# Kernel optimization log

Hardware: AMD Instinct MI355X
Metric: run time of the kernel (lower is better)

Reference implementation:

```python
import jax, jax.numpy as jnp
import numpy as np

H, HW, B, C = 8, 64, 2, 2048  # num_heads, head_width, batch, seq_len
INIT_SCALE = 0.01
C64 = jnp.complex64


def setup_inputs() -> dict:
    key = jax.random.key(0)
    ks = jax.random.split(key, 7)
    x = jax.random.normal(ks[0], (B, C, H * HW), jnp.float32)
    W_Q = jax.random.normal(ks[1], (H, HW, HW), jnp.float32) * INIT_SCALE
    W_K = jax.random.normal(ks[2], (H, HW, HW), jnp.float32) * INIT_SCALE
    W_V = jax.random.normal(ks[3], (H, HW, HW), jnp.float32) * INIT_SCALE
    theta = jax.random.normal(ks[4], (H, HW), jnp.float32) * INIT_SCALE
    # gamma schedule: 1 - 10^linspace(-6, -2, H) (non-trainable)
    log_range = jnp.arange(H, dtype=jnp.float32) / (H - 1)
    gamma = (1.0 - 10.0 ** (-6.0 + 4.0 * log_range)).astype(jnp.float32)
    target_norm = jnp.ones((H,), jnp.float32)
    qk_scale = jnp.float32(HW ** 0.5)
    W_O = jax.random.normal(ks[5], (H, HW, H * HW), jnp.float32) * INIT_SCALE
    W_G = jax.random.normal(ks[6], (H, HW, H, HW), jnp.float32) * INIT_SCALE
    return {"x": x, "W_Q": W_Q, "W_K": W_K, "W_V": W_V, "theta": theta,
            "gamma": gamma, "target_norm": target_norm, "qk_scale": qk_scale,
            "W_O": W_O, "W_G": W_G}


def reference(x, W_Q, W_K, W_V, theta, gamma, target_norm, qk_scale, W_O, W_G):
    b, c, _ = x.shape
    # decay mask D[h, i, j] = gamma_h^(i-j) for i >= j else 0
    n = jnp.arange(c, dtype=jnp.float32)
    delta = n[:, None] - n[None, :]                       # [C, C]
    causal = delta >= 0
    expo = jnp.where(causal, delta, 0.0)
    D = jnp.where(causal[None], gamma[:, None, None] ** expo[None], 0.0)  # [H,C,C]
    # complex rotary phase Theta[h, c, i] = exp(i * c * theta[h, i])
    Theta = jnp.exp(1j * n[None, :, None] * theta[:, None, :]).astype(C64)  # [H,C,HW]
    x_head = x.reshape(b, c, H, HW).astype(C64)
    Q = jnp.einsum('hij,bchi->bhcj', W_Q.astype(C64), x_head) * Theta
    K = jnp.einsum('hij,bchi->bhcj', W_K.astype(C64), x_head) * jnp.conj(Theta)
    V = jnp.einsum('hij,bchi->bhcj', W_V.astype(C64), x_head)
    QK = jnp.einsum('bhci,bhdi->bhcd', Q, K) / qk_scale.astype(C64)  # [B,H,C,C]
    QKD = QK * D.astype(C64)
    out_head = jnp.einsum('bhcd,bhdi->bchi', QKD, V)       # [B,C,H,HW]
    # per-head L2 normalization (norm of complex vector is real)
    norm = jnp.sqrt(jnp.sum(jnp.abs(out_head) ** 2, axis=-1, keepdims=True))
    out_head = out_head / norm.astype(C64)
    # NOTE: torch code computes einsum(out_head, target_norm) into a dead variable;
    # it does not affect the returned output, so it is omitted here.
    gating = jnp.einsum('bchi,hijk->bcjk', out_head, W_G.astype(C64))  # [B,C,H,HW]
    out_head = out_head * gating / (1.0 + jnp.exp(-2.0 * gating))
    output = jnp.einsum('bchi,hik->bck', out_head, W_O.astype(C64))    # [B,C,H*HW] complex
    return output
```

## Files before the change

### kernel.cpp

```cpp
#include <hip/hip_runtime.h>
#include <cstdint>
#include <cstddef>

#define B_  2
#define H_  8
#define C_  2048
#define HW_ 64
#define HD_ 512
#define N1_ 2097152

typedef __attribute__((ext_vector_type(8))) short short8;
typedef __attribute__((ext_vector_type(4))) short short4v;
typedef __attribute__((ext_vector_type(4))) float f32x4;
typedef __attribute__((ext_vector_type(4))) int   int4v;
typedef unsigned short us;

static __device__ inline us f2bf(float f) {
    unsigned u = __builtin_bit_cast(unsigned, f);
    u = u + 0x7FFFu + ((u >> 16) & 1u);
    return (us)(u >> 16);
}
static __device__ inline us f2bf_t(float f) {
    return (us)(__builtin_bit_cast(unsigned, f) >> 16);
}
static __device__ inline float bf2f(us s) {
    unsigned u = ((unsigned)s) << 16;
    return __builtin_bit_cast(float, u);
}
static __device__ inline f32x4 mfma16(short8 a, short8 b, f32x4 c) {
    return __builtin_amdgcn_mfma_f32_16x16x32_bf16(a, b, c, 0, 0, 0);
}
static __device__ inline short8 negbf(short8 v) {
    int4v u = __builtin_bit_cast(int4v, v);
    u ^= (int)0x80008000;
    return __builtin_bit_cast(short8, u);
}
static __device__ inline short8 lds_frag(const us* p) {
    short4v a = *(const short4v*)p;
    short4v b = *(const short4v*)(p + 4);
    return __builtin_shufflevector(a, b, 0, 1, 2, 3, 4, 5, 6, 7);
}
static __device__ inline short8 lds_fragg(const us* p) {
    short4v a = *(const short4v*)p;
    short4v b = *(const short4v*)(p + 16);
    return __builtin_shufflevector(a, b, 0, 1, 2, 3, 4, 5, 6, 7);
}
static __device__ inline void pkhl(float a, float b, unsigned &hw, unsigned &lw) {
    us ha = f2bf_t(a), hb = f2bf_t(b);
    hw = (unsigned)ha | ((unsigned)hb << 16);
    float la = a - bf2f(ha), lb = b - bf2f(hb);
    lw = (unsigned)f2bf_t(la) | ((unsigned)f2bf_t(lb) << 16);
}
static __device__ inline short8 bcs8(unsigned a, unsigned b, unsigned c, unsigned d) {
    int4v v = {(int)a, (int)b, (int)c, (int)d};
    return __builtin_bit_cast(short8, v);
}

__global__ __launch_bounds__(256) void proj_kernel(
    const float* __restrict__ x, const float* __restrict__ WQ,
    const float* __restrict__ WK, const float* __restrict__ WV,
    const float* __restrict__ theta,
    us* __restrict__ Qch, us* __restrict__ Qcl,
    us* __restrict__ K1h, us* __restrict__ K1l,
    us* __restrict__ VTh, us* __restrict__ VTl)
{
    __shared__ float smem[3 * 64 * 68 + 32 * 68];
    float* sWT = smem;
    float* sx  = smem + 3 * 64 * 68;
    int tid = threadIdx.x;
    int bh = blockIdx.y; int h = bh & 7;
    int c0 = blockIdx.x * 32;
    for (int t = tid; t < 1024; t += 256) {
        int j4 = (t & 15) * 4, i = t >> 4;
        float4 wq = *(const float4*)&WQ[(h * 64 + i) * 64 + j4];
        float4 wk = *(const float4*)&WK[(h * 64 + i) * 64 + j4];
        float4 wv = *(const float4*)&WV[(h * 64 + i) * 64 + j4];
        sWT[(j4 + 0) * 68 + i] = wq.x; sWT[(j4 + 1) * 68 + i] = wq.y;
        sWT[(j4 + 2) * 68 + i] = wq.z; sWT[(j4 + 3) * 68 + i] = wq.w;
        sWT[64 * 68 + (j4 + 0) * 68 + i] = wk.x; sWT[64 * 68 + (j4 + 1) * 68 + i] = wk.y;
        sWT[64 * 68 + (j4 + 2) * 68 + i] = wk.z; sWT[64 * 68 + (j4 + 3) * 68 + i] = wk.w;
        sWT[2 * 64 * 68 + (j4 + 0) * 68 + i] = wv.x; sWT[2 * 64 * 68 + (j4 + 1) * 68 + i] = wv.y;
        sWT[2 * 64 * 68 + (j4 + 2) * 68 + i] = wv.z; sWT[2 * 64 * 68 + (j4 + 3) * 68 + i] = wv.w;
    }
    for (int t = tid; t < 512; t += 256) {
        int i4 = (t & 15) * 4, c = t >> 4;
        *(float4*)&sx[c * 68 + i4] =
            *(const float4*)&x[((size_t)((bh >> 3) * C_ + c0 + c)) * HD_ + h * 64 + i4];
    }
    __syncthreads();
    int j = tid & 63, cg = tid >> 6;
    float aq[8] = {}, ak[8] = {}, av[8] = {};
    const float* pw0 = &sWT[j * 68];
    const float* pw1 = &sWT[64 * 68 + j * 68];
    const float* pw2 = &sWT[2 * 64 * 68 + j * 68];
    const float* px  = &sx[cg * 8 * 68];
    #pragma unroll 2
    for (int i0 = 0; i0 < 64; i0 += 4) {
        float4 w0 = *(const float4*)(pw0 + i0);
        float4 w1 = *(const float4*)(pw1 + i0);
        float4 w2 = *(const float4*)(pw2 + i0);
        #pragma unroll
        for (int cc = 0; cc < 8; ++cc) {
            float4 xv = *(const float4*)(px + cc * 68 + i0);
            aq[cc] += xv.x * w0.x + xv.y * w0.y + xv.z * w0.z + xv.w * w0.w;
            ak[cc] += xv.x * w1.x + xv.y * w1.y + xv.z * w1.z + xv.w * w1.w;
            av[cc] += xv.x * w2.x + xv.y * w2.y + xv.z * w2.z + xv.w * w2.w;
        }
    }
    float th = theta[h * 64 + j];
    #pragma unroll
    for (int cc = 0; cc < 8; ++cc) {
        int c = c0 + cg * 8 + cc;
        float sn, cs;
        sincosf((float)c * th, &sn, &cs);
        float qr = aq[cc] * cs, qi = aq[cc] * sn;
        float kr = ak[cc] * cs, nki = ak[cc] * sn;
        size_t rq = ((size_t)bh * C_ + c) * 128;
        us h0;
        h0 = f2bf(qr);  Qch[rq + j]      = h0; Qcl[rq + j]      = f2bf(qr  - bf2f(h0));
        h0 = f2bf(qi);  Qch[rq + 64 + j] = h0; Qcl[rq + 64 + j] = f2bf(qi  - bf2f(h0));
        h0 = f2bf(kr);  K1h[rq + j]      = h0; K1l[rq + j]      = f2bf(kr  - bf2f(h0));
        h0 = f2bf(nki); K1h[rq + 64 + j] = h0; K1l[rq + 64 + j] = f2bf(nki - bf2f(h0));
    }
    __syncthreads();
    float* T0 = smem;
    #pragma unroll
    for (int cc = 0; cc < 8; ++cc)
        T0[j * 33 + cg * 8 + cc] = av[cc];
    __syncthreads();
    int cc2 = tid & 31, jg = tid >> 5;
    #pragma unroll
    for (int jj = 0; jj < 8; ++jj) {
        int jr = jg * 8 + jj;
        float v = T0[jr * 33 + cc2];
        us hh = f2bf(v);
        size_t o = ((size_t)bh * 64 + jr) * C_ + c0 + cc2;
        VTh[o] = hh;
        VTl[o] = f2bf(v - bf2f(hh));
    }
}

__global__ __launch_bounds__(256, 3) void retention_kernel(
    const us* __restrict__ Qch, const us* __restrict__ Qcl,
    const us* __restrict__ K1h, const us* __restrict__ K1l,
    const us* __restrict__ VTh, const us* __restrict__ VTl,
    float* __restrict__ Pbuf,
    const float* __restrict__ gamma, const float* __restrict__ qk_scale)
{
    constexpr int SPV = 68;
    constexpr int SPK = 132;
    constexpr int PLV = 64 * SPV;
    constexpr int PLK = 64 * SPK;
    __shared__ us smem[2 * PLK + 2 * PLV];
    us* sKh = smem;
    us* sKl = smem + PLK;
    us* sVh = smem + 2 * PLK;
    us* sVl = smem + 2 * PLK + PLV;

    const int tid = threadIdx.x;
    const int w = tid >> 6, lane = tid & 63;
    const int ln = lane & 15, quad = lane >> 4;
    const int r = (int)blockIdx.x >> 4, bh = (int)blockIdx.x & 15;
    const int h = bh & 7;
    int qt, klo, slot;
    if (r == 0)       { qt = 15; klo = 0;  slot = 15; }
    else if (r == 1)  { qt = 31; klo = 16; slot = 47; }
    else if (r <= 17) { qt = 14 + r; klo = 0; slot = 16 + 2 * (qt - 16); }
    else {
        int u = r - 18, s = 15 - (u >> 1);
        if ((u & 1) == 0) { qt = s - 1;  klo = 0;  slot = qt; }
        else              { qt = 15 + s; klo = 16; slot = 17 + 2 * (qt - 16); }
    }
    const int khi = (qt >= 16 && klo == 0) ? 15 : qt;
    const int qc0 = qt * 64;
    const float lg = log2f(gamma[h]);
    const float inv_scale = 1.0f / qk_scale[0];
    const int qloc = w * 16 + ln;
    const float rowl = exp2f(lg * (float)qloc);
    const float e16  = exp2f(-16.0f * lg);
    float colq[4];
    #pragma unroll
    for (int r2 = 0; r2 < 4; ++r2)
        colq[r2] = exp2f(-lg * (float)(quad * 4 + r2));

    short8 Qh[4], Ql[4];
    {
        size_t qrow = ((size_t)bh * C_ + qc0 + w * 16 + ln) * 128;
        #pragma unroll
        for (int ck = 0; ck < 4; ++ck) {
            size_t off = qrow + ck * 32 + quad * 8;
            Qh[ck] = *(const short8*)(Qch + off);
            Ql[ck] = *(const short8*)(Qcl + off);
        }
    }
    f32x4 zz = {0.0f, 0.0f, 0.0f, 0.0f};
    f32x4 Or[4], Oi[4];
    #pragma unroll
    for (int it = 0; it < 4; ++it) { Or[it] = zz; Oi[it] = zz; }

    const size_t vtb = (size_t)bh * 64 * C_;
    const int krow_s = tid >> 2, kseg = (tid & 3) * 32;
    const int vi = tid >> 2, vseg = (tid & 3) * 16;

    for (int kt = klo; kt <= khi; ++kt) {
        const int kc0 = kt * 64;
        __syncthreads();
        {
            const size_t kb = ((size_t)bh * C_ + kc0 + krow_s) * 128 + kseg;
            const us* gh = K1h + kb;
            const us* gl = K1l + kb;
            us* dkh = &sKh[krow_s * SPK + kseg];
            us* dkl = &sKl[krow_s * SPK + kseg];
            #pragma unroll
            for (int m = 0; m < 4; ++m) {
                short8 a = *(const short8*)(gh + m * 8);
                *(short4v*)(dkh + m * 8)     = __builtin_shufflevector(a, a, 0, 1, 2, 3);
                *(short4v*)(dkh + m * 8 + 4) = __builtin_shufflevector(a, a, 4, 5, 6, 7);
                a = *(const short8*)(gl + m * 8);
                *(short4v*)(dkl + m * 8)     = __builtin_shufflevector(a, a, 0, 1, 2, 3);
                *(short4v*)(dkl + m * 8 + 4) = __builtin_shufflevector(a, a, 4, 5, 6, 7);
            }
            size_t g = vtb + (size_t)vi * C_ + kc0 + vseg;
            short8 a = *(const short8*)(VTh + g);
            short8 bq = *(const short8*)(VTh + g + 8);
            *(short4v*)&sVh[vi * SPV + vseg]      = __builtin_shufflevector(a, a, 0, 1, 2, 3);
            *(short4v*)&sVh[vi * SPV + vseg + 4]  = __builtin_shufflevector(a, a, 4, 5, 6, 7);
            *(short4v*)&sVh[vi * SPV + vseg + 8]  = __builtin_shufflevector(bq, bq, 0, 1, 2, 3);
            *(short4v*)&sVh[vi * SPV + vseg + 12] = __builtin_shufflevector(bq, bq, 4, 5, 6, 7);
            a  = *(const short8*)(VTl + g);
            bq = *(const short8*)(VTl + g + 8);
            *(short4v*)&sVl[vi * SPV + vseg]      = __builtin_shufflevector(a, a, 0, 1, 2, 3);
            *(short4v*)&sVl[vi * SPV + vseg + 4]  = __builtin_shufflevector(a, a, 4, 5, 6, 7);
            *(short4v*)&sVl[vi * SPV + vseg + 8]  = __builtin_shufflevector(bq, bq, 0, 1, 2, 3);
            *(short4v*)&sVl[vi * SPV + vseg + 12] = __builtin_shufflevector(bq, bq, 4, 5, 6, 7);
        }
        __syncthreads();
        const float tf = exp2f(lg * (float)(qc0 - kc0)) * inv_scale;
        const bool diag = (kt == qt);
        float snt = tf * rowl;
        #pragma unroll
        for (int half = 0; half < 2; ++half) {
            unsigned WRH[2][2], WRL[2][2], WIH[2][2], WIL[2][2];
            #pragma unroll
            for (int n2 = 0; n2 < 2; ++n2) {
                const int nt = half * 2 + n2;
                const int kr = (nt * 16 + ln) * SPK;
                short8 Kh[4], Kl[4];
                #pragma unroll
                for (int ck = 0; ck < 4; ++ck) {
                    Kh[ck] = lds_frag(&sKh[kr + ck * 32 + quad * 8]);
                    Kl[ck] = lds_frag(&sKl[kr + ck * 32 + quad * 8]);
                }
                f32x4 sr = zz, si = zz;
                #pragma unroll
                for (int ck = 0; ck < 4; ++ck) {
                    sr = mfma16(Kh[ck], Qh[ck], sr);
                    sr = mfma16(Kl[ck], Qh[ck], sr);
                    sr = mfma16(Kh[ck], Ql[ck], sr);
                }
                short8 nKh2 = negbf(Kh[2]), nKh3 = negbf(Kh[3]);
                short8 nKl2 = negbf(Kl[2]), nKl3 = negbf(Kl[3]);
                si = mfma16(nKh2, Qh[0], si); si = mfma16(nKl2, Qh[0], si); si = mfma16(nKh2, Ql[0], si);
                si = mfma16(nKh3, Qh[1], si); si = mfma16(nKl3, Qh[1], si); si = mfma16(nKh3, Ql[1], si);
                si = mfma16(Kh[0], Qh[2], si); si = mfma16(Kl[0], Qh[2], si); si = mfma16(Kh[0], Ql[2], si);
                si = mfma16(Kh[1], Qh[3], si); si = mfma16(Kl[1], Qh[3], si); si = mfma16(Kh[1], Ql[3], si);
                float ar[4], ai[4];
                #pragma unroll
                for (int r2 = 0; r2 < 4; ++r2) {
                    float wv = snt * colq[r2];
                    if (diag && (qloc < nt * 16 + quad * 4 + r2)) wv = 0.0f;
                    ar[r2] = sr[r2] * wv;
                    ai[r2] = si[r2] * wv;
                }
                pkhl(ar[0], ar[1], WRH[n2][0], WRL[n2][0]);
                pkhl(ar[2], ar[3], WRH[n2][1], WRL[n2][1]);
                pkhl(ai[0], ai[1], WIH[n2][0], WIL[n2][0]);
                pkhl(ai[2], ai[3], WIH[n2][1], WIL[n2][1]);
                snt *= e16;
            }
            short8 SRH = bcs8(WRH[0][0], WRH[0][1], WRH[1][0], WRH[1][1]);
            short8 SRL = bcs8(WRL[0][0], WRL[0][1], WRL[1][0], WRL[1][1]);
            short8 SIH = bcs8(WIH[0][0], WIH[0][1], WIH[1][0], WIH[1][1]);
            short8 SIL = bcs8(WIL[0][0], WIL[0][1], WIL[1][0], WIL[1][1]);
            #pragma unroll
            for (int it = 0; it < 4; ++it) {
                int vb = (it * 16 + ln) * SPV + half * 32 + quad * 4;
                short8 Vh = lds_fragg(&sVh[vb]);
                short8 Vl = lds_fragg(&sVl[vb]);
                Or[it] = mfma16(SRH, Vh, Or[it]);
                Or[it] = mfma16(SRH, Vl, Or[it]);
                Or[it] = mfma16(SRL, Vh, Or[it]);
                Oi[it] = mfma16(SIH, Vh, Oi[it]);
                Oi[it] = mfma16(SIH, Vl, Oi[it]);
                Oi[it] = mfma16(SIL, Vh, Oi[it]);
            }
        }
    }
    float* Pr = Pbuf + ((size_t)(bh * 48 + slot)) * 8192;
    float* Pi = Pr + 4096;
    #pragma unroll
    for (int it = 0; it < 4; ++it) {
        #pragma unroll
        for (int rr2 = 0; rr2 < 4; ++rr2) {
            int qL = w * 16 + quad * 4 + rr2, iX = it * 16 + ln;
            Pr[qL * 64 + iX] = Or[it][rr2];
            Pi[qL * 64 + iX] = Oi[it][rr2];
        }
    }
}

__global__ __launch_bounds__(256) void reduce_wcvt_kernel(
    const float* __restrict__ Pbuf,
    us* __restrict__ A1h, us* __restrict__ A1l,
    const float* __restrict__ WG, const float* __restrict__ WO,
    us* __restrict__ Gh, us* __restrict__ Gl,
    us* __restrict__ Oh, us* __restrict__ Ol)
{
    __shared__ float T[32 * 33];
    if ((int)blockIdx.x < 32) {
        const int qt = blockIdx.x, bh = blockIdx.y;
        const int h = bh & 7, b = bh >> 3;
        const int t = threadIdx.x;
        const int q = t >> 2, i0 = (t & 3) * 16;
        const int slot0 = (qt < 16) ? qt : 16 + 2 * (qt - 16);
        const int nparts = (qt < 16) ? 1 : 2;
        const float* P0 = Pbuf + ((size_t)(bh * 48 + slot0)) * 8192 + q * 64 + i0;
        float orv[16], oiv[16];
        #pragma unroll
        for (int s4 = 0; s4 < 4; ++s4) {
            *(float4*)&orv[s4 * 4] = *(const float4*)(P0 + s4 * 4);
            *(float4*)&oiv[s4 * 4] = *(const float4*)(P0 + 4096 + s4 * 4);
        }
        if (nparts == 2) {
            const float* P1 = P0 + 8192;
            #pragma unroll
            for (int s4 = 0; s4 < 4; ++s4) {
                float4 a = *(const float4*)(P1 + s4 * 4);
                float4 c = *(const float4*)(P1 + 4096 + s4 * 4);
                orv[s4 * 4]     += a.x; orv[s4 * 4 + 1] += a.y;
                orv[s4 * 4 + 2] += a.z; orv[s4 * 4 + 3] += a.w;
                oiv[s4 * 4]     += c.x; oiv[s4 * 4 + 1] += c.y;
                oiv[s4 * 4 + 2] += c.z; oiv[s4 * 4 + 3] += c.w;
            }
        }
        float ss = 0.0f;
        #pragma unroll
        for (int k = 0; k < 16; ++k) ss += orv[k] * orv[k] + oiv[k] * oiv[k];
        ss += __shfl_xor(ss, 1);
        ss += __shfl_xor(ss, 2);
        float rn = rsqrtf(ss);
        size_t o = (((size_t)(b * C_ + qt * 64 + q)) * H_ + h) * HW_ + i0;
        us th[16], tl[16];
        #pragma unroll
        for (int k = 0; k < 16; ++k) {
            float v = orv[k] * rn;
            us hh = f2bf(v); th[k] = hh; tl[k] = f2bf(v - bf2f(hh));
        }
        *(short8*)&A1h[o] = *(short8*)&th[0]; *(short8*)&A1h[o + 8] = *(short8*)&th[8];
        *(short8*)&A1l[o] = *(short8*)&tl[0]; *(short8*)&A1l[o + 8] = *(short8*)&tl[8];
        #pragma unroll
        for (int k = 0; k < 16; ++k) {
            float v = oiv[k] * rn;
            us hh = f2bf(v); th[k] = hh; tl[k] = f2bf(v - bf2f(hh));
        }
        *(short8*)&A1h[N1_ + o] = *(short8*)&th[0]; *(short8*)&A1h[N1_ + o + 8] = *(short8*)&th[8];
        *(short8*)&A1l[N1_ + o] = *(short8*)&tl[0]; *(short8*)&A1l[N1_ + o + 8] = *(short8*)&tl[8];
    } else {
        int widx = ((int)blockIdx.x - 32) * 16 + (int)blockIdx.y;
        int z = widx >> 8, w2 = widx & 255;
        const float* src = z ? WO : WG;
        us* dh = z ? Oh : Gh;
        us* dl = z ? Ol : Gl;
        int k0 = (w2 >> 4) * 32, n0 = (w2 & 15) * 32;
        int c = threadIdx.x & 31, r8 = threadIdx.x >> 5;
        #pragma unroll
        for (int rr = 0; rr < 4; ++rr) {
            int rw = r8 * 4 + rr;
            T[rw * 33 + c] = src[(size_t)(k0 + rw) * 512 + n0 + c];
        }
        __syncthreads();
        #pragma unroll
        for (int rr = 0; rr < 4; ++rr) {
            int rw = r8 * 4 + rr;
            float v = T[c * 33 + rw];
            us hh = f2bf(v);
            size_t o = (size_t)(n0 + rw) * 512 + k0 + c;
            dh[o] = hh; dl[o] = f2bf(v - bf2f(hh));
        }
    }
}

__global__ __launch_bounds__(256) void gemm_gate_kernel(
    const us* __restrict__ Ah, const us* __restrict__ Al,
    const us* __restrict__ BTh, const us* __restrict__ BTl,
    us* __restrict__ A2h, us* __restrict__ A2l)
{
    constexpr int SPB = 132;
    constexpr int PLB = 64 * SPB;
    __shared__ us sB[2 * PLB];
    us* sBh = sB;
    us* sBl = sB + PLB;
    const int tid = threadIdx.x;
    const int w = tid >> 6, lane = tid & 63;
    const int ln = lane & 15, quad = lane >> 4;
    const int bm = blockIdx.x * 64 + w * 16;
    const int bn = blockIdx.y * 64;
    const int brow = tid >> 2, bseg = (tid & 3) * 32;
    f32x4 accR[4], accI[4];
    #pragma unroll
    for (int nt = 0; nt < 4; ++nt) {
        accR[nt] = (f32x4){0.f, 0.f, 0.f, 0.f};
        accI[nt] = (f32x4){0.f, 0.f, 0.f, 0.f};
    }
    const us* pAr[2];
    const us* pAi[2];
    {
        size_t rr = (size_t)(bm + ln) * 512 + quad * 8;
        pAr[0] = Ah + rr;        pAr[1] = Al + rr;
        pAi[0] = Ah + N1_ + rr;  pAi[1] = Al + N1_ + rr;
    }
    for (int kc = 0; kc < 4; ++kc) {
        const int kc0 = kc * 128;
        __syncthreads();
        {
            const size_t gb = (size_t)(bn + brow) * 512 + kc0 + bseg;
            us* dh = &sBh[brow * SPB + bseg];
            us* dl = &sBl[brow * SPB + bseg];
            #pragma unroll
            for (int m = 0; m < 4; ++m) {
                short8 a = *(const short8*)(BTh + gb + m * 8);
                *(short4v*)(dh + m * 8)     = __builtin_shufflevector(a, a, 0, 1, 2, 3);
                *(short4v*)(dh + m * 8 + 4) = __builtin_shufflevector(a, a, 4, 5, 6, 7);
                a = *(const short8*)(BTl + gb + m * 8);
                *(short4v*)(dl + m * 8)     = __builtin_shufflevector(a, a, 0, 1, 2, 3);
                *(short4v*)(dl + m * 8 + 4) = __builtin_shufflevector(a, a, 4, 5, 6, 7);
            }
        }
        __syncthreads();
        #pragma unroll
        for (int ks = 0; ks < 4; ++ks) {
            const int ko = kc0 + ks * 32;
            const int lo = ks * 32 + quad * 8;
            short8 Ar[2], Ai[2], Bf[4][2];
            Ar[0] = *(const short8*)(pAr[0] + ko);
            Ar[1] = *(const short8*)(pAr[1] + ko);
            Ai[0] = *(const short8*)(pAi[0] + ko);
            Ai[1] = *(const short8*)(pAi[1] + ko);
            #pragma unroll
            for (int nt = 0; nt < 4; ++nt) {
                Bf[nt][0] = lds_frag(&sBh[(nt * 16 + ln) * SPB + lo]);
                Bf[nt][1] = lds_frag(&sBl[(nt * 16 + ln) * SPB + lo]);
            }
            #pragma unroll
            for (int nt = 0; nt < 4; ++nt) {
                accR[nt] = mfma16(Ar[0], Bf[nt][0], accR[nt]);
                accR[nt] = mfma16(Ar[0], Bf[nt][1], accR[nt]);
                accR[nt] = mfma16(Ar[1], Bf[nt][0], accR[nt]);
                accI[nt] = mfma16(Ai[0], Bf[nt][0], accI[nt]);
                accI[nt] = mfma16(Ai[0], Bf[nt][1], accI[nt]);
                accI[nt] = mfma16(Ai[1], Bf[nt][0], accI[nt]);
            }
        }
    }
    #pragma unroll
    for (int nt = 0; nt < 4; ++nt)
        #pragma unroll
        for (int r = 0; r < 4; ++r) {
            int m = bm + quad * 4 + r;
            int n = bn + nt * 16 + ln;
            size_t idx = (size_t)m * 512 + n;
            float gr = accR[nt][r], gi = accI[nt][r];
            float hr = bf2f(Ah[idx]) + bf2f(Al[idx]);
            float hi = bf2f(Ah[N1_ + idx]) + bf2f(Al[N1_ + idx]);
            float e = __expf(-2.0f * gr);
            float sn, cs;
            __sincosf(2.0f * gi, &sn, &cs);
            float dr = 1.0f + e * cs;
            float di = -e * sn;
            float nr = hr * gr - hi * gi;
            float ni = hr * gi + hi * gr;
            float inv = 1.0f / (dr * dr + di * di);
            float o2r = (nr * dr + ni * di) * inv;
            float o2i = (ni * dr - nr * di) * inv;
            us t = f2bf(o2r);
            A2h[idx] = t; A2l[idx] = f2bf(o2r - bf2f(t));
            t = f2bf(o2i);
            A2h[N1_ + idx] = t; A2l[N1_ + idx] = f2bf(o2i - bf2f(t));
        }
}

__global__ __launch_bounds__(256) void gemm_mfma_kernel(
    const us* __restrict__ Ah, const us* __restrict__ Al,
    const us* __restrict__ BTh, const us* __restrict__ BTl,
    float* __restrict__ Cout, int mode)
{
    constexpr int SPB = 132;
    constexpr int PLB = 64 * SPB;
    __shared__ us sB[2 * PLB];
    us* sBh = sB;
    us* sBl = sB + PLB;
    const int tid = threadIdx.x;
    const int w = tid >> 6, lane = tid & 63;
    const int ln = lane & 15, quad = lane >> 4;
    const int bm = blockIdx.x * 64 + w * 16;
    const int bn = blockIdx.y * 64;
    const int brow = tid >> 2, bseg = (tid & 3) * 32;
    f32x4 acc[4];
    #pragma unroll
    for (int nt = 0; nt < 4; ++nt) acc[nt] = (f32x4){0.f, 0.f, 0.f, 0.f};
    const us* pA[2];
    {
        size_t r = (size_t)(bm + ln) * 512 + quad * 8;
        pA[0] = Ah + r; pA[1] = Al + r;
    }
    for (int kc = 0; kc < 4; ++kc) {
        const int kc0 = kc * 128;
        __syncthreads();
        {
            const size_t gb = (size_t)(bn + brow) * 512 + kc0 + bseg;
            us* dh = &sBh[brow * SPB + bseg];
            us* dl = &sBl[brow * SPB + bseg];
            #pragma unroll
            for (int m = 0; m < 4; ++m) {
                short8 a = *(const short8*)(BTh + gb + m * 8);
                *(short4v*)(dh + m * 8)     = __builtin_shufflevector(a, a, 0, 1, 2, 3);
                *(short4v*)(dh + m * 8 + 4) = __builtin_shufflevector(a, a, 4, 5, 6, 7);
                a = *(const short8*)(BTl + gb + m * 8);
                *(short4v*)(dl + m * 8)     = __builtin_shufflevector(a, a, 0, 1, 2, 3);
                *(short4v*)(dl + m * 8 + 4) = __builtin_shufflevector(a, a, 4, 5, 6, 7);
            }
        }
        __syncthreads();
        #pragma unroll
        for (int ks = 0; ks < 4; ++ks) {
            const int ko = kc0 + ks * 32;
            const int lo = ks * 32 + quad * 8;
            short8 Af[2], Bf[4][2];
            Af[0] = *(const short8*)(pA[0] + ko);
            Af[1] = *(const short8*)(pA[1] + ko);
            #pragma unroll
            for (int nt = 0; nt < 4; ++nt) {
                Bf[nt][0] = lds_frag(&sBh[(nt * 16 + ln) * SPB + lo]);
                Bf[nt][1] = lds_frag(&sBl[(nt * 16 + ln) * SPB + lo]);
            }
            #pragma unroll
            for (int nt = 0; nt < 4; ++nt) {
                acc[nt] = mfma16(Af[0], Bf[nt][0], acc[nt]);
                acc[nt] = mfma16(Af[0], Bf[nt][1], acc[nt]);
                acc[nt] = mfma16(Af[1], Bf[nt][0], acc[nt]);
            }
        }
    }
    #pragma unroll
    for (int nt = 0; nt < 4; ++nt)
        #pragma unroll
        for (int r = 0; r < 4; ++r) {
            int m = bm + quad * 4 + r;
            int n = bn + nt * 16 + ln;
            float v = acc[nt][r];
            if (mode == 0) {
                Cout[(size_t)m * 512 + n] = v;
            } else if (mode == 1) {
                if (m < 4096) Cout[2 * ((size_t)m * 512 + n)] = v;
                else          Cout[2 * ((size_t)(m - 4096) * 512 + n) + 1] = v;
            } else {
                if (m < 4096) Cout[(size_t)m * 512 + n] = v;
            }
        }
}

extern "C" void kernel_launch(void* const* d_in, const int* in_sizes, int n_in,
                              void* d_out, int out_size, void* d_ws, size_t ws_size,
                              hipStream_t stream)
{
    const float* x     = (const float*)d_in[0];
    const float* WQ    = (const float*)d_in[1];
    const float* WK    = (const float*)d_in[2];
    const float* WV    = (const float*)d_in[3];
    const float* theta = (const float*)d_in[4];
    const float* gamma = (const float*)d_in[5];
    const float* qk    = (const float*)d_in[7];
    const float* WO    = (const float*)d_in[8];
    const float* WG    = (const float*)d_in[9];
    float* out = (float*)d_out;

    const size_t N1 = (size_t)B_ * H_ * C_ * HW_;
    const size_t SQ = (size_t)B_ * H_ * C_ * 128;
    const size_t SV = (size_t)B_ * H_ * HW_ * C_;
    us* usw = (us*)d_ws;
    us *Qch = usw,            *Qcl = usw + SQ,
       *K1h = usw + 2 * SQ,   *K1l = usw + 3 * SQ,
       *VTh = usw + 4 * SQ,   *VTl = usw + 4 * SQ + SV;
    float* fw = (float*)d_ws;
    us *A1h = (us*)(fw + 5 * N1), *A1l = (us*)(fw + 6 * N1);
    us *WTGh = K1h,            *WTGl = K1h + 262144,
       *WTOh = K1h + 524288,  *WTOl = K1h + 786432;
    us *A2h = (us*)(fw + 9 * N1), *A2l = (us*)(fw + 10 * N1);
    float *Pbuf = fw + 7 * N1;

    proj_kernel<<<dim3(C_ / 32, B_ * H_), 256, 0, stream>>>(
        x, WQ, WK, WV, theta, Qch, Qcl, K1h, K1l, VTh, VTl);
    retention_kernel<<<dim3(768), 256, 0, stream>>>(
        Qch, Qcl, K1h, K1l, VTh, VTl, Pbuf, gamma, qk);
    reduce_wcvt_kernel<<<dim3(64, 16), 256, 0, stream>>>(
        Pbuf, A1h, A1l, WG, WO, WTGh, WTGl, WTOh, WTOl);

    gemm_gate_kernel<<<dim3(64, 8), 256, 0, stream>>>(
        A1h, A1l, WTGh, WTGl, A2h, A2l);

    int outmode = (out_size >= (int)(2 * N1)) ? 1 : 2;
    gemm_mfma_kernel<<<dim3(128, 8), 256, 0, stream>>>(
        A2h, A2l, WTOh, WTOl, out, outmode);
}
```

Before: 252.9 us.

## Split retention key range into 8-tile chunks and halve K shared-memory staging

```diff
diff --git a/kernel.cpp b/kernel.cpp
--- a/kernel.cpp
+++ b/kernel.cpp
@@ -8,6 +8,7 @@
 #define HW_ 64
 #define HD_ 512
 #define N1_ 2097152
+#define NSLOT_ 80
 
 typedef __attribute__((ext_vector_type(8))) short short8;
 typedef __attribute__((ext_vector_type(4))) short short4v;
@@ -108,11 +109,13 @@
         }
     }
     float th = theta[h * 64 + j];
+    float ths, thc;
+    sincosf(th, &ths, &thc);
+    float sn, cs;
+    sincosf((float)(c0 + cg * 8) * th, &sn, &cs);
     #pragma unroll
     for (int cc = 0; cc < 8; ++cc) {
         int c = c0 + cg * 8 + cc;
-        float sn, cs;
-        sincosf((float)c * th, &sn, &cs);
         float qr = aq[cc] * cs, qi = aq[cc] * sn;
         float kr = ak[cc] * cs, nki = ak[cc] * sn;
         size_t rq = ((size_t)bh * C_ + c) * 128;
@@ -121,6 +124,9 @@
         h0 = f2bf(qi);  Qch[rq + 64 + j] = h0; Qcl[rq + 64 + j] = f2bf(qi  - bf2f(h0));
         h0 = f2bf(kr);  K1h[rq + j]      = h0; K1l[rq + j]      = f2bf(kr  - bf2f(h0));
         h0 = f2bf(nki); K1h[rq + 64 + j] = h0; K1l[rq + 64 + j] = f2bf(nki - bf2f(h0));
+        float ncs = cs * thc - sn * ths;
+        float nsn = sn * thc + cs * ths;
+        cs = ncs; sn = nsn;
     }
     __syncthreads();
     float* T0 = smem;
@@ -140,7 +146,7 @@
     }
 }
 
-__global__ __launch_bounds__(256, 3) void retention_kernel(
+__global__ __launch_bounds__(256, 4) void retention_kernel(
     const us* __restrict__ Qch, const us* __restrict__ Qcl,
     const us* __restrict__ K1h, const us* __restrict__ K1l,
     const us* __restrict__ VTh, const us* __restrict__ VTl,
@@ -150,28 +156,32 @@
     constexpr int SPV = 68;
     constexpr int SPK = 132;
     constexpr int PLV = 64 * SPV;
-    constexpr int PLK = 64 * SPK;
-    __shared__ us smem[2 * PLK + 2 * PLV];
+    constexpr int PLKH = 32 * SPK;
+    __shared__ us smem[2 * PLKH + 2 * PLV];
     us* sKh = smem;
-    us* sKl = smem + PLK;
-    us* sVh = smem + 2 * PLK;
-    us* sVl = smem + 2 * PLK + PLV;
+    us* sKl = smem + PLKH;
+    us* sVh = smem + 2 * PLKH;
+    us* sVl = smem + 2 * PLKH + PLV;
 
     const int tid = threadIdx.x;
     const int w = tid >> 6, lane = tid & 63;
     const int ln = lane & 15, quad = lane >> 4;
-    const int r = (int)blockIdx.x >> 4, bh = (int)blockIdx.x & 15;
+    const int bi = (int)blockIdx.x;
+    const int bh = 2 * (bi & 7) + ((bi >> 3) & 1);
+    const int r  = bi >> 4;
     const int h = bh & 7;
-    int qt, klo, slot;
-    if (r == 0)       { qt = 15; klo = 0;  slot = 15; }
-    else if (r == 1)  { qt = 31; klo = 16; slot = 47; }
-    else if (r <= 17) { qt = 14 + r; klo = 0; slot = 16 + 2 * (qt - 16); }
-    else {
-        int u = r - 18, s = 15 - (u >> 1);
-        if ((u & 1) == 0) { qt = s - 1;  klo = 0;  slot = qt; }
-        else              { qt = 15 + s; klo = 16; slot = 17 + 2 * (qt - 16); }
-    }
-    const int khi = (qt >= 16 && klo == 0) ? 15 : qt;
+    int qt, j;
+    if (r < 8)       { qt = r;                    j = 0; }
+    else if (r < 24) { qt = 8  + ((r - 8) >> 1);  j = (r - 8) & 1; }
+    else if (r < 48) { qt = 16 + (r - 24) / 3;    j = (r - 24) % 3; }
+    else             { qt = 24 + ((r - 48) >> 2); j = (r - 48) & 3; }
+    const int klo = 8 * j;
+    const int khi = (klo + 7 < qt) ? klo + 7 : qt;
+    const int base = (qt < 8) ? qt
+                   : (qt < 16) ? 8  + 2 * (qt - 8)
+                   : (qt < 24) ? 24 + 3 * (qt - 16)
+                   :             48 + 4 * (qt - 24);
+    const int slot = base + j;
     const int qc0 = qt * 64;
     const float lg = log2f(gamma[h]);
     const float inv_scale = 1.0f / qk_scale[0];
@@ -199,52 +209,52 @@
     for (int it = 0; it < 4; ++it) { Or[it] = zz; Oi[it] = zz; }
 
     const size_t vtb = (size_t)bh * 64 * C_;
-    const int krow_s = tid >> 2, kseg = (tid & 3) * 32;
+    const int krow_h = tid >> 3, kseg_h = (tid & 7) * 16;
     const int vi = tid >> 2, vseg = (tid & 3) * 16;
 
     for (int kt = klo; kt <= khi; ++kt) {
         const int kc0 = kt * 64;
-        __syncthreads();
-        {
-            const size_t kb = ((size_t)bh * C_ + kc0 + krow_s) * 128 + kseg;
-            const us* gh = K1h + kb;
-            const us* gl = K1l + kb;
-            us* dkh = &sKh[krow_s * SPK + kseg];
-            us* dkl = &sKl[krow_s * SPK + kseg];
-            #pragma unroll
-            for (int m = 0; m < 4; ++m) {
-                short8 a = *(const short8*)(gh + m * 8);
-                *(short4v*)(dkh + m * 8)     = __builtin_shufflevector(a, a, 0, 1, 2, 3);
-                *(short4v*)(dkh + m * 8 + 4) = __builtin_shufflevector(a, a, 4, 5, 6, 7);
-                a = *(const short8*)(gl + m * 8);
-                *(short4v*)(dkl + m * 8)     = __builtin_shufflevector(a, a, 0, 1, 2, 3);
-                *(short4v*)(dkl + m * 8 + 4) = __builtin_shufflevector(a, a, 4, 5, 6, 7);
-            }
-            size_t g = vtb + (size_t)vi * C_ + kc0 + vseg;
-            short8 a = *(const short8*)(VTh + g);
-            short8 bq = *(const short8*)(VTh + g + 8);
-            *(short4v*)&sVh[vi * SPV + vseg]      = __builtin_shufflevector(a, a, 0, 1, 2, 3);
-            *(short4v*)&sVh[vi * SPV + vseg + 4]  = __builtin_shufflevector(a, a, 4, 5, 6, 7);
-            *(short4v*)&sVh[vi * SPV + vseg + 8]  = __builtin_shufflevector(bq, bq, 0, 1, 2, 3);
-            *(short4v*)&sVh[vi * SPV + vseg + 12] = __builtin_shufflevector(bq, bq, 4, 5, 6, 7);
-            a  = *(const short8*)(VTl + g);
-            bq = *(const short8*)(VTl + g + 8);
-            *(short4v*)&sVl[vi * SPV + vseg]      = __builtin_shufflevector(a, a, 0, 1, 2, 3);
-            *(short4v*)&sVl[vi * SPV + vseg + 4]  = __builtin_shufflevector(a, a, 4, 5, 6, 7);
-            *(short4v*)&sVl[vi * SPV + vseg + 8]  = __builtin_shufflevector(bq, bq, 0, 1, 2, 3);
-            *(short4v*)&sVl[vi * SPV + vseg + 12] = __builtin_shufflevector(bq, bq, 4, 5, 6, 7);
-        }
-        __syncthreads();
         const float tf = exp2f(lg * (float)(qc0 - kc0)) * inv_scale;
         const bool diag = (kt == qt);
         float snt = tf * rowl;
         #pragma unroll
         for (int half = 0; half < 2; ++half) {
+            __syncthreads();
+            {
+                const size_t kb = ((size_t)bh * C_ + kc0 + half * 32 + krow_h) * 128 + kseg_h;
+                us* dkh = &sKh[krow_h * SPK + kseg_h];
+                us* dkl = &sKl[krow_h * SPK + kseg_h];
+                #pragma unroll
+                for (int m = 0; m < 2; ++m) {
+                    short8 a = *(const short8*)(K1h + kb + m * 8);
+                    *(short4v*)(dkh + m * 8)     = __builtin_shufflevector(a, a, 0, 1, 2, 3);
+                    *(short4v*)(dkh + m * 8 + 4) = __builtin_shufflevector(a, a, 4, 5, 6, 7);
+                    a = *(const short8*)(K1l + kb + m * 8);
+                    *(short4v*)(dkl + m * 8)     = __builtin_shufflevector(a, a, 0, 1, 2, 3);
+                    *(short4v*)(dkl + m * 8 + 4) = __builtin_shufflevector(a, a, 4, 5, 6, 7);
+                }
+                if (half == 0) {
+                    size_t g = vtb + (size_t)vi * C_ + kc0 + vseg;
+                    short8 a = *(const short8*)(VTh + g);
+                    short8 bq = *(const short8*)(VTh + g + 8);
+                    *(short4v*)&sVh[vi * SPV + vseg]      = __builtin_shufflevector(a, a, 0, 1, 2, 3);
+                    *(short4v*)&sVh[vi * SPV + vseg + 4]  = __builtin_shufflevector(a, a, 4, 5, 6, 7);
+                    *(short4v*)&sVh[vi * SPV + vseg + 8]  = __builtin_shufflevector(bq, bq, 0, 1, 2, 3);
+                    *(short4v*)&sVh[vi * SPV + vseg + 12] = __builtin_shufflevector(bq, bq, 4, 5, 6, 7);
+                    a  = *(const short8*)(VTl + g);
+                    bq = *(const short8*)(VTl + g + 8);
+                    *(short4v*)&sVl[vi * SPV + vseg]      = __builtin_shufflevector(a, a, 0, 1, 2, 3);
+                    *(short4v*)&sVl[vi * SPV + vseg + 4]  = __builtin_shufflevector(a, a, 4, 5, 6, 7);
+                    *(short4v*)&sVl[vi * SPV + vseg + 8]  = __builtin_shufflevector(bq, bq, 0, 1, 2, 3);
+                    *(short4v*)&sVl[vi * SPV + vseg + 12] = __builtin_shufflevector(bq, bq, 4, 5, 6, 7);
+                }
+            }
+            __syncthreads();
             unsigned WRH[2][2], WRL[2][2], WIH[2][2], WIL[2][2];
             #pragma unroll
             for (int n2 = 0; n2 < 2; ++n2) {
                 const int nt = half * 2 + n2;
-                const int kr = (nt * 16 + ln) * SPK;
+                const int kr = (n2 * 16 + ln) * SPK;
                 short8 Kh[4], Kl[4];
                 #pragma unroll
                 for (int ck = 0; ck < 4; ++ck) {
@@ -296,7 +306,7 @@
             }
         }
     }
-    float* Pr = Pbuf + ((size_t)(bh * 48 + slot)) * 8192;
+    float* Pr = Pbuf + ((size_t)(bh * NSLOT_ + slot)) * 8192;
     float* Pi = Pr + 4096;
     #pragma unroll
     for (int it = 0; it < 4; ++it) {
@@ -322,17 +332,20 @@
         const int h = bh & 7, b = bh >> 3;
         const int t = threadIdx.x;
         const int q = t >> 2, i0 = (t & 3) * 16;
-        const int slot0 = (qt < 16) ? qt : 16 + 2 * (qt - 16);
-        const int nparts = (qt < 16) ? 1 : 2;
-        const float* P0 = Pbuf + ((size_t)(bh * 48 + slot0)) * 8192 + q * 64 + i0;
+        const int np = (qt >> 3) + 1;
+        const int slot0 = (qt < 8) ? qt
+                        : (qt < 16) ? 8  + 2 * (qt - 8)
+                        : (qt < 24) ? 24 + 3 * (qt - 16)
+                        :             48 + 4 * (qt - 24);
+        const float* P0 = Pbuf + ((size_t)(bh * NSLOT_ + slot0)) * 8192 + q * 64 + i0;
         float orv[16], oiv[16];
         #pragma unroll
         for (int s4 = 0; s4 < 4; ++s4) {
             *(float4*)&orv[s4 * 4] = *(const float4*)(P0 + s4 * 4);
             *(float4*)&oiv[s4 * 4] = *(const float4*)(P0 + 4096 + s4 * 4);
         }
-        if (nparts == 2) {
-            const float* P1 = P0 + 8192;
+        for (int pp = 1; pp < np; ++pp) {
+            const float* P1 = P0 + (size_t)pp * 8192;
             #pragma unroll
             for (int s4 = 0; s4 < 4; ++s4) {
                 float4 a = *(const float4*)(P1 + s4 * 4);
@@ -592,15 +605,15 @@
        *K1h = usw + 2 * SQ,   *K1l = usw + 3 * SQ,
        *VTh = usw + 4 * SQ,   *VTl = usw + 4 * SQ + SV;
     float* fw = (float*)d_ws;
-    us *A1h = (us*)(fw + 5 * N1), *A1l = (us*)(fw + 6 * N1);
-    us *WTGh = K1h,            *WTGl = K1h + 262144,
+    float *Pbuf = fw + 5 * N1;
+    us *A1h = usw,            *A1l = usw + SQ;
+    us *WTGh = K1h,           *WTGl = K1h + 262144,
        *WTOh = K1h + 524288,  *WTOl = K1h + 786432;
-    us *A2h = (us*)(fw + 9 * N1), *A2l = (us*)(fw + 10 * N1);
-    float *Pbuf = fw + 7 * N1;
+    us *A2h = (us*)(fw + 5 * N1), *A2l = (us*)(fw + 6 * N1);
 
     proj_kernel<<<dim3(C_ / 32, B_ * H_), 256, 0, stream>>>(
         x, WQ, WK, WV, theta, Qch, Qcl, K1h, K1l, VTh, VTl);
-    retention_kernel<<<dim3(768), 256, 0, stream>>>(
+    retention_kernel<<<dim3(1280), 256, 0, stream>>>(
         Qch, Qcl, K1h, K1l, VTh, VTl, Pbuf, gamma, qk);
     reduce_wcvt_kernel<<<dim3(64, 16), 256, 0, stream>>>(
         Pbuf, A1h, A1l, WG, WO, WTGh, WTGl, WTOh, WTOl);
```

New measurement: 399.5 us. 1.58x slower.
